# Kernel optimization log

Hardware: AMD Instinct MI355X
Metric: run time of the kernel (lower is better)

Reference implementation:

```python
import jax, jax.numpy as jnp
import numpy as np

N_NODES = 100000
N_EDGES = 1600000
D = 64  # latent = hidden = output = 64


def gcn_conv(x, W, b, src, dst, n):
    # PyG GCNConv: out = D^{-1/2} (A + I) D^{-1/2} (x W) + b, self-loops added.
    h = x @ W  # [N, d_out]
    ones = jnp.ones(src.shape[0], dtype=h.dtype)
    deg = jax.ops.segment_sum(ones, dst, num_segments=n) + 1.0  # +1 for self-loop
    dinv = jax.lax.rsqrt(deg)  # [N]
    norm = dinv[src] * dinv[dst]  # [E]
    msgs = h[src] * norm[:, None]  # gather + scale, [E, d_out]
    agg = jax.ops.segment_sum(msgs, dst, num_segments=n)  # scatter-add
    # self-loop contribution: dinv[i]^2 * h[i]
    agg = agg + h * (dinv * dinv)[:, None]
    return agg + b


def setup_inputs() -> dict:
    key = jax.random.key(0)
    ks = jax.random.split(key, 9)
    s = 1.0 / np.sqrt(D)
    return {
        "z": jax.random.normal(ks[0], (N_NODES, D), dtype=jnp.float32),
        "src": jax.random.randint(ks[1], (N_EDGES,), 0, N_NODES, dtype=jnp.int32),
        "dst": jax.random.randint(ks[2], (N_EDGES,), 0, N_NODES, dtype=jnp.int32),
        "W1": jax.random.uniform(ks[3], (D, D), jnp.float32, -s, s),
        "b1": jnp.zeros((D,), jnp.float32),
        "W2": jax.random.uniform(ks[4], (D, D), jnp.float32, -s, s),
        "b2": jnp.zeros((D,), jnp.float32),
        "W3": jax.random.uniform(ks[5], (D, D), jnp.float32, -s, s),
        "b3": jnp.zeros((D,), jnp.float32),
    }


def reference(z, src, dst, W1, b1, W2, b2, W3, b3):
    n = z.shape[0]
    x = jax.nn.relu(gcn_conv(z, W1, b1, src, dst, n))
    x = jax.nn.relu(gcn_conv(x, W2, b2, src, dst, n))
    x = gcn_conv(x, W3, b3, src, dst, n)
    return x
```

## Files before the change

kernel.cpp:

```cpp
#include <hip/hip_runtime.h>
#include <hip/hip_fp16.h>

#define N_NODES 100000
#define N_EDGES 1600000
#define N_BUCKETS 256
#define BUCKET_NODES 391
#define BKT_BLOCKS 512
#define CAP_E 8192
#define CAP_C 12288
#define DUMMY N_NODES

typedef unsigned short u16;
typedef _Float16 f16x8 __attribute__((ext_vector_type(8)));
typedef float f32x4 __attribute__((ext_vector_type(4)));

__device__ __forceinline__ u16 f2h(float f) {
    return __half_as_ushort(__float2half_rn(f));
}

__device__ __forceinline__ void acc8(float* acc, uint4 q) {
    unsigned v[4] = {q.x, q.y, q.z, q.w};
#pragma unroll
    for (int i = 0; i < 4; ++i) {
        __half2 h = *reinterpret_cast<__half2*>(&v[i]);
        float2 f = __half22float2(h);
        acc[2 * i] += f.x;
        acc[2 * i + 1] += f.y;
    }
}

__global__ __launch_bounds__(256) void k_bucket(const int* __restrict__ src,
                                                const int* __restrict__ dst,
                                                int* __restrict__ btot,
                                                int* __restrict__ ebuf) {
    __shared__ int cnt[N_BUCKETS], base_s[N_BUCKETS];
    const int CS = N_EDGES / BKT_BLOCKS;
    int t = threadIdx.x;
    int beg = blockIdx.x * CS, end = beg + CS;
    for (int i = t; i < N_BUCKETS; i += 256) cnt[i] = 0;
    __syncthreads();
    for (int e = beg + t; e < end; e += 256)
        atomicAdd(&cnt[(unsigned)dst[e] / BUCKET_NODES], 1);
    __syncthreads();
    for (int i = t; i < N_BUCKETS; i += 256) {
        base_s[i] = atomicAdd(&btot[i], cnt[i]);
        cnt[i] = 0;
    }
    __syncthreads();
    for (int e = beg + t; e < end; e += 256) {
        int d = dst[e], s = src[e];
        int b = (unsigned)d / BUCKET_NODES;
        int l = atomicAdd(&cnt[b], 1);
        ebuf[b * CAP_E + base_s[b] + l] = s | ((d - b * BUCKET_NODES) << 17);
    }
}

__global__ __launch_bounds__(1024) void k_build(const int* __restrict__ btot,
                                                const int* __restrict__ ebuf,
                                                int* __restrict__ col,
                                                int2* __restrict__ rowinfo,
                                                float* __restrict__ dinv,
                                                const float* __restrict__ z,
                                                u16* __restrict__ xs,
                                                u16* __restrict__ xs_other) {
    __shared__ int deg[BUCKET_NODES];
    __shared__ int cur[BUCKET_NODES];
    __shared__ int sm[512];
    __shared__ int cls[CAP_C];
    int b = blockIdx.x, t = threadIdx.x;
    int nb = b * BUCKET_NODES;
    int nn = N_NODES - nb < BUCKET_NODES ? N_NODES - nb : BUCKET_NODES;
    int ne = btot[b];
    const int* eb = ebuf + b * CAP_E;

    for (int i = t; i < BUCKET_NODES; i += 1024) deg[i] = 0;
    __syncthreads();
    for (int e = t; e < ne; e += 1024) atomicAdd(&deg[eb[e] >> 17], 1);
    __syncthreads();

    int v = (t < nn) ? ((deg[t] + 7) & ~7) : 0;
    if (t < 512) sm[t] = v;
    __syncthreads();
    for (int off = 1; off < 512; off <<= 1) {
        int u = (t >= off && t < 512) ? sm[t - off] : 0;
        __syncthreads();
        if (t < 512) sm[t] += u;
        __syncthreads();
    }
    int total = sm[511];
    int colbase = b * CAP_C;
    if (t < nn) {
        int off0 = sm[t] - v;
        cur[t] = off0;
        rowinfo[nb + t] = make_int2(colbase + off0, v);
        dinv[nb + t] = rsqrtf((float)deg[t] + 1.0f);
    }
    __syncthreads();
    for (int i = t; i < total; i += 1024) cls[i] = DUMMY << 7;
    __syncthreads();
    for (int e = t; e < ne; e += 1024) {
        int pe = eb[e];
        int l = atomicAdd(&cur[pe >> 17], 1);
        cls[l] = (pe & 0x1FFFF) << 7;
    }
    __syncthreads();
    for (int i = t; i < total; i += 1024) col[colbase + i] = cls[i];
    if (t < 16) col[colbase + total + t] = DUMMY << 7;

    const float4* zz = (const float4*)(z + (size_t)nb * 64);
    uint2* xx = (uint2*)(xs + (size_t)nb * 64);
    for (int i = t; i < nn * 16; i += 1024) {
        float4 vv = zz[i];
        float dd = rsqrtf((float)deg[i >> 4] + 1.0f);
        unsigned p0 = (unsigned)f2h(vv.x * dd) | ((unsigned)f2h(vv.y * dd) << 16);
        unsigned p1 = (unsigned)f2h(vv.z * dd) | ((unsigned)f2h(vv.w * dd) << 16);
        xx[i] = make_uint2(p0, p1);
    }
    if (b == 0 && t < 8) {
        ((uint4*)(xs + (size_t)N_NODES * 64))[t] = make_uint4(0, 0, 0, 0);
        ((uint4*)(xs_other + (size_t)N_NODES * 64))[t] = make_uint4(0, 0, 0, 0);
    }
}

__global__ __launch_bounds__(256, 4) void k_agg(const int2* __restrict__ rowinfo,
                                                const int* __restrict__ col,
                                                const float* __restrict__ dinv,
                                                const u16* __restrict__ xs,
                                                u16* __restrict__ h) {
    const int lane = threadIdx.x & 63;
    const int eighth = lane >> 3;
    const int fh = lane & 7;
    const char* xb = (const char*)xs;
    int wave = (blockIdx.x * blockDim.x + threadIdx.x) >> 6;
    int nwaves = (gridDim.x * blockDim.x) >> 6;

    for (int n0 = wave * 2; n0 < N_NODES; n0 += nwaves * 2) {
        int u0 = __builtin_amdgcn_readfirstlane(n0);
        int u1 = u0 + 1;
        bool has1 = (u1 < N_NODES);
        int2 r0 = rowinfo[u0];
        int2 r1 = has1 ? rowinfo[u1] : r0;
        int it0 = r0.y >> 4, it1 = r1.y >> 4;
        int itm = it0 > it1 ? it0 : it1;

        uint4 qs0 = *(const uint4*)(xb + (size_t)u0 * 128 + fh * 16);
        uint4 qs1 = *(const uint4*)(xb + (size_t)u1 * 128 + fh * 16);
        float d0 = dinv[u0];
        float d1 = has1 ? dinv[u1] : 0.f;

        float a0[8] = {0.f, 0.f, 0.f, 0.f, 0.f, 0.f, 0.f, 0.f};
        float a1[8] = {0.f, 0.f, 0.f, 0.f, 0.f, 0.f, 0.f, 0.f};
        for (int r = 0; r < itm; r += 2) {
            int rb = r + 1;
            int oa0 = (r  < it0) ? (r  << 4) : 0;
            int oa1 = (r  < it1) ? (r  << 4) : 0;
            int ob0 = (rb < it0) ? (rb << 4) : 0;
            int ob1 = (rb < it1) ? (rb << 4) : 0;
            int2 ca = *(const int2*)(col + r0.x + oa0 + 2 * eighth);
            int2 cb = *(const int2*)(col + r1.x + oa1 + 2 * eighth);
            int2 cc = *(const int2*)(col + r0.x + ob0 + 2 * eighth);
            int2 cd = *(const int2*)(col + r1.x + ob1 + 2 * eighth);
            uint4 qa = *(const uint4*)(xb + (unsigned)ca.x + fh * 16);
            uint4 qb = *(const uint4*)(xb + (unsigned)ca.y + fh * 16);
            uint4 qc = *(const uint4*)(xb + (unsigned)cb.x + fh * 16);
            uint4 qd = *(const uint4*)(xb + (unsigned)cb.y + fh * 16);
            uint4 qe = *(const uint4*)(xb + (unsigned)cc.x + fh * 16);
            uint4 qf = *(const uint4*)(xb + (unsigned)cc.y + fh * 16);
            uint4 qg = *(const uint4*)(xb + (unsigned)cd.x + fh * 16);
            uint4 qh = *(const uint4*)(xb + (unsigned)cd.y + fh * 16);
            if (r  < it0) { acc8(a0, qa); acc8(a0, qb); }
            if (r  < it1) { acc8(a1, qc); acc8(a1, qd); }
            if (rb < it0) { acc8(a0, qe); acc8(a0, qf); }
            if (rb < it1) { acc8(a1, qg); acc8(a1, qh); }
        }
        int t0 = (r0.y >> 3) & 1, t1 = (r1.y >> 3) & 1;
        if (t0 | t1) {
            int s0 = col[r0.x + (it0 << 4) + eighth];
            int s1 = col[r1.x + (it1 << 4) + eighth];
            uint4 q0 = *(const uint4*)(xb + (unsigned)s0 + fh * 16);
            uint4 q1 = *(const uint4*)(xb + (unsigned)s1 + fh * 16);
            if (t0) acc8(a0, q0);
            if (t1) acc8(a1, q1);
        }

#pragma unroll
        for (int m = 8; m <= 32; m <<= 1) {
#pragma unroll
            for (int j = 0; j < 8; ++j) {
                a0[j] += __shfl_xor(a0[j], m, 64);
                a1[j] += __shfl_xor(a1[j], m, 64);
            }
        }
        float s0[8] = {0.f, 0.f, 0.f, 0.f, 0.f, 0.f, 0.f, 0.f};
        float s1[8] = {0.f, 0.f, 0.f, 0.f, 0.f, 0.f, 0.f, 0.f};
        acc8(s0, qs0); acc8(s1, qs1);
        uint4 p0, p1;
        u16* pp0 = (u16*)&p0;
        u16* pp1 = (u16*)&p1;
#pragma unroll
        for (int j = 0; j < 8; ++j) {
            pp0[j] = f2h((a0[j] + s0[j]) * d0);
            pp1[j] = f2h((a1[j] + s1[j]) * d1);
        }
        if (eighth == 0) ((uint4*)(h + (size_t)u0 * 64))[fh] = p0;
        if (has1 && eighth == 1) ((uint4*)(h + (size_t)u1 * 64))[fh] = p1;
    }
}

__global__ __launch_bounds__(256) void k_mv(const u16* __restrict__ h,
                                            const float* __restrict__ W,
                                            const float* __restrict__ bias,
                                            const float* __restrict__ dinv,
                                            u16* __restrict__ outh,
                                            float* __restrict__ outf, int hidden) {
    const int lane = threadIdx.x & 63;
    const int quad = lane >> 4;
    const int l16 = lane & 15;

    f16x8 bfr[4][2];
#pragma unroll
    for (int t = 0; t < 4; ++t)
#pragma unroll
        for (int c = 0; c < 2; ++c)
#pragma unroll
            for (int j = 0; j < 8; ++j)
                bfr[t][c][j] = (_Float16)W[(quad * 8 + 32 * c + j) * 64 + 4 * l16 + t];
    float bv[4];
#pragma unroll
    for (int t = 0; t < 4; ++t) bv[t] = bias[4 * l16 + t];

    int wave = (blockIdx.x * blockDim.x + threadIdx.x) >> 6;
    int nwaves = (gridDim.x * blockDim.x) >> 6;
    for (int chunk = wave; chunk < N_NODES / 16; chunk += nwaves) {
        int row0 = chunk * 16;
        const u16* hb = h + (size_t)row0 * 64;
        union { uint4 u; f16x8 f; } a0, a1;
        a0.u = *(const uint4*)(hb + l16 * 64 + quad * 8);
        a1.u = *(const uint4*)(hb + l16 * 64 + quad * 8 + 32);

        f32x4 acc[4] = {{0.f, 0.f, 0.f, 0.f}, {0.f, 0.f, 0.f, 0.f},
                        {0.f, 0.f, 0.f, 0.f}, {0.f, 0.f, 0.f, 0.f}};
#pragma unroll
        for (int t = 0; t < 4; ++t) {
            acc[t] = __builtin_amdgcn_mfma_f32_16x16x32_f16(a0.f, bfr[t][0], acc[t], 0, 0, 0);
            acc[t] = __builtin_amdgcn_mfma_f32_16x16x32_f16(a1.f, bfr[t][1], acc[t], 0, 0, 0);
        }
        float dv[4];
#pragma unroll
        for (int r = 0; r < 4; ++r) dv[r] = dinv[row0 + quad * 4 + r];
#pragma unroll
        for (int r = 0; r < 4; ++r) {
            int row = row0 + quad * 4 + r;
            float o[4];
#pragma unroll
            for (int t = 0; t < 4; ++t) o[t] = acc[t][r] + bv[t];
            if (hidden) {
                float dd = dv[r];
#pragma unroll
                for (int t = 0; t < 4; ++t) o[t] = fmaxf(o[t], 0.f) * dd;
                unsigned lo = (unsigned)f2h(o[0]) | ((unsigned)f2h(o[1]) << 16);
                unsigned hi = (unsigned)f2h(o[2]) | ((unsigned)f2h(o[3]) << 16);
                ((uint2*)(outh + (size_t)row * 64))[l16] = make_uint2(lo, hi);
            } else {
                ((float4*)(outf + (size_t)row * 64))[l16] =
                    make_float4(o[0], o[1], o[2], o[3]);
            }
        }
    }
}

extern "C" void kernel_launch(void* const* d_in, const int* in_sizes, int n_in,
                              void* d_out, int out_size, void* d_ws, size_t ws_size,
                              hipStream_t stream) {
    const float* z  = (const float*)d_in[0];
    const int* src  = (const int*)d_in[1];
    const int* dst  = (const int*)d_in[2];
    const float* W1 = (const float*)d_in[3];
    const float* b1 = (const float*)d_in[4];
    const float* W2 = (const float*)d_in[5];
    const float* b2 = (const float*)d_in[6];
    const float* W3 = (const float*)d_in[7];
    const float* b3 = (const float*)d_in[8];
    float* out = (float*)d_out;

    char* p = (char*)d_ws;
    float* dinv    = (float*)p;  p += (size_t)512 << 10;
    int2*  rowinfo = (int2*)p;   p += (size_t)1 << 20;
    int*   btot    = (int*)p;    p += (size_t)4 << 10;
    int*   ebuf    = (int*)p;    p += (size_t)N_BUCKETS * CAP_E * 4;
    int*   col     = (int*)p;    p += (size_t)N_BUCKETS * CAP_C * 4;
    u16*   hbuf    = (u16*)p;    p += (size_t)13 << 20;
    u16*   buf0    = (u16*)p;    p += (size_t)13 << 20;
    u16*   buf1    = (u16*)p;

    const int gA = 2048;
    const int gM = 512;

    hipMemsetAsync(btot, 0, N_BUCKETS * sizeof(int), stream);
    k_bucket<<<BKT_BLOCKS, 256, 0, stream>>>(src, dst, btot, ebuf);
    k_build<<<N_BUCKETS, 1024, 0, stream>>>(btot, ebuf, col, rowinfo, dinv, z, buf0, buf1);

    k_agg<<<gA, 256, 0, stream>>>(rowinfo, col, dinv, buf0, hbuf);
    k_mv <<<gM, 256, 0, stream>>>(hbuf, W1, b1, dinv, buf1, nullptr, 1);
    k_agg<<<gA, 256, 0, stream>>>(rowinfo, col, dinv, buf1, hbuf);
    k_mv <<<gM, 256, 0, stream>>>(hbuf, W2, b2, dinv, buf0, nullptr, 1);
    k_agg<<<gA, 256, 0, stream>>>(rowinfo, col, dinv, buf0, hbuf);
    k_mv <<<gM, 256, 0, stream>>>(hbuf, W3, b3, dinv, nullptr, out, 0);
}
```

Baseline: 288.4 us.

## Process four nodes per wave in aggregation with prefetched column indices; prepack weights

The aggregation kernel now handles four destination nodes per wave instead of two. It software-pipelines the column-index loads for the next iteration while the current neighbour rows are gathered, with sched_barriers to keep loads issued ahead of the accumulation, and it folds the self-loop term into the accumulator before the cross-lane reduction. A new small kernel pre-converts and pre-swizzles the three weight matrices into fp16 MFMA fragment layout, so the matmul kernel loads them as uint4 instead of doing scalar strided loads and conversions, and the matmul grid is enlarged. The main aim is more memory-level parallelism in the gather. The cost is higher register pressure from four accumulators, and the removed tail guard relies on N_NODES being divisible by 4.

```diff
diff --git a/kernel.cpp b/kernel.cpp
--- a/kernel.cpp
+++ b/kernel.cpp
@@ -134,54 +134,71 @@
     int wave = (blockIdx.x * blockDim.x + threadIdx.x) >> 6;
     int nwaves = (gridDim.x * blockDim.x) >> 6;
 
-    for (int n0 = wave * 2; n0 < N_NODES; n0 += nwaves * 2) {
+    for (int n0 = wave * 4; n0 < N_NODES; n0 += nwaves * 4) {
         int u0 = __builtin_amdgcn_readfirstlane(n0);
-        int u1 = u0 + 1;
-        bool has1 = (u1 < N_NODES);
         int2 r0 = rowinfo[u0];
-        int2 r1 = has1 ? rowinfo[u1] : r0;
-        int it0 = r0.y >> 4, it1 = r1.y >> 4;
+        int2 r1 = rowinfo[u0 + 1];
+        int2 r2 = rowinfo[u0 + 2];
+        int2 r3 = rowinfo[u0 + 3];
+        int it0 = r0.y >> 4, it1 = r1.y >> 4, it2 = r2.y >> 4, it3 = r3.y >> 4;
         int itm = it0 > it1 ? it0 : it1;
-
-        uint4 qs0 = *(const uint4*)(xb + (size_t)u0 * 128 + fh * 16);
-        uint4 qs1 = *(const uint4*)(xb + (size_t)u1 * 128 + fh * 16);
-        float d0 = dinv[u0];
-        float d1 = has1 ? dinv[u1] : 0.f;
+        if (it2 > itm) itm = it2;
+        if (it3 > itm) itm = it3;
+
+        int2 c0 = *(const int2*)(col + r0.x + 2 * eighth);
+        int2 c1 = *(const int2*)(col + r1.x + 2 * eighth);
+        int2 c2 = *(const int2*)(col + r2.x + 2 * eighth);
+        int2 c3 = *(const int2*)(col + r3.x + 2 * eighth);
+        int tc0 = col[r0.x + (it0 << 4) + eighth];
+        int tc1 = col[r1.x + (it1 << 4) + eighth];
+        int tc2 = col[r2.x + (it2 << 4) + eighth];
+        int tc3 = col[r3.x + (it3 << 4) + eighth];
+        uint4 s0 = *(const uint4*)(xb + (size_t)u0 * 128 + fh * 16);
+        uint4 s1 = *(const uint4*)(xb + (size_t)(u0 + 1) * 128 + fh * 16);
+        uint4 s2 = *(const uint4*)(xb + (size_t)(u0 + 2) * 128 + fh * 16);
+        uint4 s3 = *(const uint4*)(xb + (size_t)(u0 + 3) * 128 + fh * 16);
 
         float a0[8] = {0.f, 0.f, 0.f, 0.f, 0.f, 0.f, 0.f, 0.f};
         float a1[8] = {0.f, 0.f, 0.f, 0.f, 0.f, 0.f, 0.f, 0.f};
-        for (int r = 0; r < itm; r += 2) {
-            int rb = r + 1;
-            int oa0 = (r  < it0) ? (r  << 4) : 0;
-            int oa1 = (r  < it1) ? (r  << 4) : 0;
-            int ob0 = (rb < it0) ? (rb << 4) : 0;
-            int ob1 = (rb < it1) ? (rb << 4) : 0;
-            int2 ca = *(const int2*)(col + r0.x + oa0 + 2 * eighth);
-            int2 cb = *(const int2*)(col + r1.x + oa1 + 2 * eighth);
-            int2 cc = *(const int2*)(col + r0.x + ob0 + 2 * eighth);
-            int2 cd = *(const int2*)(col + r1.x + ob1 + 2 * eighth);
-            uint4 qa = *(const uint4*)(xb + (unsigned)ca.x + fh * 16);
-            uint4 qb = *(const uint4*)(xb + (unsigned)ca.y + fh * 16);
-            uint4 qc = *(const uint4*)(xb + (unsigned)cb.x + fh * 16);
-            uint4 qd = *(const uint4*)(xb + (unsigned)cb.y + fh * 16);
-            uint4 qe = *(const uint4*)(xb + (unsigned)cc.x + fh * 16);
-            uint4 qf = *(const uint4*)(xb + (unsigned)cc.y + fh * 16);
-            uint4 qg = *(const uint4*)(xb + (unsigned)cd.x + fh * 16);
-            uint4 qh = *(const uint4*)(xb + (unsigned)cd.y + fh * 16);
-            if (r  < it0) { acc8(a0, qa); acc8(a0, qb); }
-            if (r  < it1) { acc8(a1, qc); acc8(a1, qd); }
-            if (rb < it0) { acc8(a0, qe); acc8(a0, qf); }
-            if (rb < it1) { acc8(a1, qg); acc8(a1, qh); }
-        }
-        int t0 = (r0.y >> 3) & 1, t1 = (r1.y >> 3) & 1;
-        if (t0 | t1) {
-            int s0 = col[r0.x + (it0 << 4) + eighth];
-            int s1 = col[r1.x + (it1 << 4) + eighth];
-            uint4 q0 = *(const uint4*)(xb + (unsigned)s0 + fh * 16);
-            uint4 q1 = *(const uint4*)(xb + (unsigned)s1 + fh * 16);
-            if (t0) acc8(a0, q0);
-            if (t1) acc8(a1, q1);
-        }
+        float a2[8] = {0.f, 0.f, 0.f, 0.f, 0.f, 0.f, 0.f, 0.f};
+        float a3[8] = {0.f, 0.f, 0.f, 0.f, 0.f, 0.f, 0.f, 0.f};
+
+        for (int rr = 0; rr < itm; ++rr) {
+            uint4 q0 = *(const uint4*)(xb + (unsigned)c0.x + fh * 16);
+            uint4 q1 = *(const uint4*)(xb + (unsigned)c0.y + fh * 16);
+            uint4 q2 = *(const uint4*)(xb + (unsigned)c1.x + fh * 16);
+            uint4 q3 = *(const uint4*)(xb + (unsigned)c1.y + fh * 16);
+            uint4 q4 = *(const uint4*)(xb + (unsigned)c2.x + fh * 16);
+            uint4 q5 = *(const uint4*)(xb + (unsigned)c2.y + fh * 16);
+            uint4 q6 = *(const uint4*)(xb + (unsigned)c3.x + fh * 16);
+            uint4 q7 = *(const uint4*)(xb + (unsigned)c3.y + fh * 16);
+            int rn = rr + 1;
+            if (rn < itm) {
+                c0 = *(const int2*)(col + r0.x + ((rn < it0 ? rn : 0) << 4) + 2 * eighth);
+                c1 = *(const int2*)(col + r1.x + ((rn < it1 ? rn : 0) << 4) + 2 * eighth);
+                c2 = *(const int2*)(col + r2.x + ((rn < it2 ? rn : 0) << 4) + 2 * eighth);
+                c3 = *(const int2*)(col + r3.x + ((rn < it3 ? rn : 0) << 4) + 2 * eighth);
+            }
+            __builtin_amdgcn_sched_barrier(0);
+            if (rr < it0) { acc8(a0, q0); acc8(a0, q1); }
+            if (rr < it1) { acc8(a1, q2); acc8(a1, q3); }
+            if (rr < it2) { acc8(a2, q4); acc8(a2, q5); }
+            if (rr < it3) { acc8(a3, q6); acc8(a3, q7); }
+        }
+
+        uint4 g0 = *(const uint4*)(xb + (unsigned)tc0 + fh * 16);
+        uint4 g1 = *(const uint4*)(xb + (unsigned)tc1 + fh * 16);
+        uint4 g2 = *(const uint4*)(xb + (unsigned)tc2 + fh * 16);
+        uint4 g3 = *(const uint4*)(xb + (unsigned)tc3 + fh * 16);
+        __builtin_amdgcn_sched_barrier(0);
+        if ((r0.y >> 3) & 1) acc8(a0, g0);
+        if ((r1.y >> 3) & 1) acc8(a1, g1);
+        if ((r2.y >> 3) & 1) acc8(a2, g2);
+        if ((r3.y >> 3) & 1) acc8(a3, g3);
+        if (eighth == 0) acc8(a0, s0);
+        if (eighth == 1) acc8(a1, s1);
+        if (eighth == 2) acc8(a2, s2);
+        if (eighth == 3) acc8(a3, s3);
 
 #pragma unroll
         for (int m = 8; m <= 32; m <<= 1) {
@@ -189,26 +206,48 @@
             for (int j = 0; j < 8; ++j) {
                 a0[j] += __shfl_xor(a0[j], m, 64);
                 a1[j] += __shfl_xor(a1[j], m, 64);
+                a2[j] += __shfl_xor(a2[j], m, 64);
+                a3[j] += __shfl_xor(a3[j], m, 64);
             }
         }
-        float s0[8] = {0.f, 0.f, 0.f, 0.f, 0.f, 0.f, 0.f, 0.f};
-        float s1[8] = {0.f, 0.f, 0.f, 0.f, 0.f, 0.f, 0.f, 0.f};
-        acc8(s0, qs0); acc8(s1, qs1);
-        uint4 p0, p1;
+        float d0 = dinv[u0];
+        float d1 = dinv[u0 + 1];
+        float d2 = dinv[u0 + 2];
+        float d3 = dinv[u0 + 3];
+        uint4 p0, p1, p2, p3;
         u16* pp0 = (u16*)&p0;
         u16* pp1 = (u16*)&p1;
+        u16* pp2 = (u16*)&p2;
+        u16* pp3 = (u16*)&p3;
 #pragma unroll
         for (int j = 0; j < 8; ++j) {
-            pp0[j] = f2h((a0[j] + s0[j]) * d0);
-            pp1[j] = f2h((a1[j] + s1[j]) * d1);
+            pp0[j] = f2h(a0[j] * d0);
+            pp1[j] = f2h(a1[j] * d1);
+            pp2[j] = f2h(a2[j] * d2);
+            pp3[j] = f2h(a3[j] * d3);
         }
         if (eighth == 0) ((uint4*)(h + (size_t)u0 * 64))[fh] = p0;
-        if (has1 && eighth == 1) ((uint4*)(h + (size_t)u1 * 64))[fh] = p1;
+        if (eighth == 1) ((uint4*)(h + (size_t)(u0 + 1) * 64))[fh] = p1;
+        if (eighth == 2) ((uint4*)(h + (size_t)(u0 + 2) * 64))[fh] = p2;
+        if (eighth == 3) ((uint4*)(h + (size_t)(u0 + 3) * 64))[fh] = p3;
+    }
+}
+
+__global__ __launch_bounds__(256) void k_prepw(const float* __restrict__ W1,
+                                               const float* __restrict__ W2,
+                                               const float* __restrict__ W3,
+                                               u16* __restrict__ Wp) {
+    const float* W = blockIdx.x == 0 ? W1 : (blockIdx.x == 1 ? W2 : W3);
+    u16* o = Wp + blockIdx.x * 4096;
+    for (int f = threadIdx.x; f < 4096; f += 256) {
+        int j = f & 7, l16 = (f >> 3) & 15, quad = (f >> 7) & 3;
+        int c = (f >> 9) & 1, t = f >> 10;
+        o[f] = f2h(W[(quad * 8 + 32 * c + j) * 64 + 4 * l16 + t]);
     }
 }
 
 __global__ __launch_bounds__(256) void k_mv(const u16* __restrict__ h,
-                                            const float* __restrict__ W,
+                                            const u16* __restrict__ Wp,
                                             const float* __restrict__ bias,
                                             const float* __restrict__ dinv,
                                             u16* __restrict__ outh,
@@ -217,17 +256,15 @@
     const int quad = lane >> 4;
     const int l16 = lane & 15;
 
-    f16x8 bfr[4][2];
+    const uint4* wq = (const uint4*)Wp;
+    union { uint4 u; f16x8 f; } bfr[4][2];
 #pragma unroll
     for (int t = 0; t < 4; ++t)
 #pragma unroll
         for (int c = 0; c < 2; ++c)
-#pragma unroll
-            for (int j = 0; j < 8; ++j)
-                bfr[t][c][j] = (_Float16)W[(quad * 8 + 32 * c + j) * 64 + 4 * l16 + t];
-    float bv[4];
-#pragma unroll
-    for (int t = 0; t < 4; ++t) bv[t] = bias[4 * l16 + t];
+            bfr[t][c].u = wq[t * 128 + c * 64 + quad * 16 + l16];
+    float4 bq = ((const float4*)bias)[l16];
+    float bv[4] = {bq.x, bq.y, bq.z, bq.w};
 
     int wave = (blockIdx.x * blockDim.x + threadIdx.x) >> 6;
     int nwaves = (gridDim.x * blockDim.x) >> 6;
@@ -242,8 +279,8 @@
                         {0.f, 0.f, 0.f, 0.f}, {0.f, 0.f, 0.f, 0.f}};
 #pragma unroll
         for (int t = 0; t < 4; ++t) {
-            acc[t] = __builtin_amdgcn_mfma_f32_16x16x32_f16(a0.f, bfr[t][0], acc[t], 0, 0, 0);
-            acc[t] = __builtin_amdgcn_mfma_f32_16x16x32_f16(a1.f, bfr[t][1], acc[t], 0, 0, 0);
+            acc[t] = __builtin_amdgcn_mfma_f32_16x16x32_f16(a0.f, bfr[t][0].f, acc[t], 0, 0, 0);
+            acc[t] = __builtin_amdgcn_mfma_f32_16x16x32_f16(a1.f, bfr[t][1].f, acc[t], 0, 0, 0);
         }
         float dv[4];
 #pragma unroll
@@ -291,19 +328,21 @@
     int*   col     = (int*)p;    p += (size_t)N_BUCKETS * CAP_C * 4;
     u16*   hbuf    = (u16*)p;    p += (size_t)13 << 20;
     u16*   buf0    = (u16*)p;    p += (size_t)13 << 20;
-    u16*   buf1    = (u16*)p;
+    u16*   buf1    = (u16*)p;    p += (size_t)13 << 20;
+    u16*   wp      = (u16*)p;
 
     const int gA = 2048;
-    const int gM = 512;
-
+    const int gM = 1563;
+
+    k_prepw<<<3, 256, 0, stream>>>(W1, W2, W3, wp);
     hipMemsetAsync(btot, 0, N_BUCKETS * sizeof(int), stream);
     k_bucket<<<BKT_BLOCKS, 256, 0, stream>>>(src, dst, btot, ebuf);
     k_build<<<N_BUCKETS, 1024, 0, stream>>>(btot, ebuf, col, rowinfo, dinv, z, buf0, buf1);
 
     k_agg<<<gA, 256, 0, stream>>>(rowinfo, col, dinv, buf0, hbuf);
-    k_mv <<<gM, 256, 0, stream>>>(hbuf, W1, b1, dinv, buf1, nullptr, 1);
+    k_mv <<<gM, 256, 0, stream>>>(hbuf, wp, b1, dinv, buf1, nullptr, 1);
     k_agg<<<gA, 256, 0, stream>>>(rowinfo, col, dinv, buf1, hbuf);
-    k_mv <<<gM, 256, 0, stream>>>(hbuf, W2, b2, dinv, buf0, nullptr, 1);
+    k_mv <<<gM, 256, 0, stream>>>(hbuf, wp + 4096, b2, dinv, buf0, nullptr, 1);
     k_agg<<<gA, 256, 0, stream>>>(rowinfo, col, dinv, buf0, hbuf);
-    k_mv <<<gM, 256, 0, stream>>>(hbuf, W3, b3, dinv, nullptr, out, 0);
-}
+    k_mv <<<gM, 256, 0, stream>>>(hbuf, wp + 8192, b3, dinv, nullptr, out, 0);
+}
```

Result: faster. 261.3 us (-9.4%).
